# Kernel tuning notes

Hardware: AMD Instinct MI355X
Metric: run time of the kernel (lower is better)

Reference implementation:

```python
import jax, jax.numpy as jnp
import numpy as np

N_WIRES = 8
EMBED = 768
B, S = 16, 2048


def setup_inputs() -> dict:
    key = jax.random.key(0)
    k1, k2, k3, k4 = jax.random.split(key, 4)
    return {
        "x": jax.random.normal(k1, (B, S, EMBED), dtype=jnp.float32),
        "w_q": jax.random.normal(k2, (N_WIRES, EMBED), dtype=jnp.float32) * (1.0 / np.sqrt(EMBED)),
        "w_out": jax.random.normal(k3, (EMBED, N_WIRES), dtype=jnp.float32) * (1.0 / np.sqrt(N_WIRES)),
        "q_params": jax.random.normal(k4, (N_WIRES,), dtype=jnp.float32),
    }


def _simulate(angles):
    """Statevector sim: RX(angle_w) on each wire w, then ring of CNOTs, then <Z_w>.
    angles: [B, S, n].  Returns [B, S, n] Pauli-Z expectations."""
    b, s, n = angles.shape
    # |0...0> initial state, one qubit per trailing axis of size 2
    state = jnp.zeros((b, s) + (2,) * n, dtype=jnp.complex64)
    state = state.at[(slice(None), slice(None)) + (0,) * n].set(1.0)
    # RX gates (data angle + learned angle already fused in `angles`)
    for w in range(n):
        ax = 2 + w
        half = angles[..., w] * 0.5
        bshape = (b, s) + (1,) * (n - 1)
        c = jnp.cos(half).reshape(bshape)
        si = jnp.sin(half).reshape(bshape)
        a0 = jnp.take(state, 0, axis=ax)
        a1 = jnp.take(state, 1, axis=ax)
        state = jnp.stack([c * a0 - 1j * si * a1, -1j * si * a0 + c * a1], axis=ax)
    # CNOT chain: (0,1),(1,2),...,(n-2,n-1),(n-1,0)
    for src, tgt in [(i, i + 1) for i in range(n - 1)] + [(n - 1, 0)]:
        sax, tax = 2 + src, 2 + tgt
        a0 = jnp.take(state, 0, axis=sax)
        a1 = jnp.take(state, 1, axis=sax)
        tadj = tax - (1 if tax > sax else 0)  # target axis after removing src axis
        state = jnp.stack([a0, jnp.flip(a1, axis=tadj)], axis=sax)
    probs = jnp.real(state * jnp.conj(state))  # [B,S,2,...,2]
    zs = []
    for w in range(n):
        axes = tuple(a for a in range(2, 2 + n) if a != 2 + w)
        marg = probs.sum(axis=axes)  # [B,S,2]
        zs.append(marg[..., 0] - marg[..., 1])
    return jnp.stack(zs, axis=-1)


def reference(x, w_q, w_out, q_params):
    # per-token RX angles; two RX on same wire commute -> fuse data + learned angle
    angles = jnp.einsum("bse,ne->bsn", x, w_q) + q_params  # [B,S,n]
    z = _simulate(angles)  # [B,S,n]
    return jnp.einsum("bsn,en->bse", z, w_out)  # [B,S,E]
```

## Files before the change

kernel.cpp:

```cpp
#include <hip/hip_runtime.h>
#include <math.h>


using f32x4 = __attribute__((ext_vector_type(4))) float;

constexpr int E  = 768;
constexpr int NW = 8;
constexpr int BLOCK = 256;
constexpr int TOKENS = 16 * 2048;
constexpr int TOK_PER_WAVE  = 4;
constexpr int TOK_PER_BLOCK = TOK_PER_WAVE * 4;
constexpr int GRID = TOKENS / TOK_PER_BLOCK;

__device__ __forceinline__ float dot12(const f32x4& a0, const f32x4& a1, const f32x4& a2,
                                       const f32x4& b0, const f32x4& b1, const f32x4& b2) {
    return a0.x*b0.x + a0.y*b0.y + a0.z*b0.z + a0.w*b0.w
         + a1.x*b1.x + a1.y*b1.y + a1.z*b1.z + a1.w*b1.w
         + a2.x*b2.x + a2.y*b2.y + a2.z*b2.z + a2.w*b2.w;
}

__device__ __forceinline__ void circuit8(const float zf[NW], int lane, float qpl,
                                         float z[NW]) {
    float v4[4];
    #pragma unroll
    for (int i = 0; i < 4; ++i) {
        float a = zf[2*i], b = zf[2*i+1];
        float keep = (lane & 1) ? b : a;
        float send = (lane & 1) ? a : b;
        v4[i] = keep + __shfl_xor(send, 1, 64);
    }
    float v2[2];
    #pragma unroll
    for (int i = 0; i < 2; ++i) {
        float a = v4[2*i], b = v4[2*i+1];
        float keep = (lane & 2) ? b : a;
        float send = (lane & 2) ? a : b;
        v2[i] = keep + __shfl_xor(send, 2, 64);
    }
    float a = v2[0], b = v2[1];
    float keep = (lane & 4) ? b : a;
    float send = (lane & 4) ? a : b;
    float v = keep + __shfl_xor(send, 4, 64);
    v += __shfl_xor(v, 8, 64);
    v += __shfl_xor(v, 16, 64);
    v += __shfl_xor(v, 32, 64);
    float c = __cosf(v + qpl);
    float cx = __shfl_xor(c, 1, 64);
    float e0 = (lane & 1) ? cx : c;
    float e1 = (lane & 1) ? c : cx;
    float e0x = __shfl_xor(e0, 2, 64), e1x = __shfl_xor(e1, 2, 64);
    float f0 = (lane & 2) ? e0x : e0;
    float f1 = (lane & 2) ? e1x : e1;
    float f2 = (lane & 2) ? e0  : e0x;
    float f3 = (lane & 2) ? e1  : e1x;
    float f0x = __shfl_xor(f0, 4, 64), f1x = __shfl_xor(f1, 4, 64);
    float f2x = __shfl_xor(f2, 4, 64), f3x = __shfl_xor(f3, 4, 64);
    float c0 = (lane & 4) ? f0x : f0;
    float c1 = (lane & 4) ? f1x : f1;
    float c2 = (lane & 4) ? f2x : f2;
    float c3 = (lane & 4) ? f3x : f3;
    float c4 = (lane & 4) ? f0  : f0x;
    float c5 = (lane & 4) ? f1  : f1x;
    float c6 = (lane & 4) ? f2  : f2x;
    float c7 = (lane & 4) ? f3  : f3x;
    float p1 = c0*c1, p2 = p1*c2, p3 = p2*c3, p4 = p3*c4;
    float p5 = p4*c5, p6 = p5*c6, p7 = p6*c7;
    float s  = c1*c2*c3*c4*c5*c6*c7;
    z[0] = s;  z[1] = p1; z[2] = p2; z[3] = p3;
    z[4] = p4; z[5] = p5; z[6] = p6; z[7] = p7;
}

__global__ __launch_bounds__(BLOCK, 4)
void mhaq_kernel(const float* __restrict__ x,
                 const float* __restrict__ w_q,
                 const float* __restrict__ w_out,
                 const float* __restrict__ q_params,
                 float* __restrict__ out)
{
    __shared__ float wq_lds[NW][E];
    __shared__ float wt_lds[NW][E];

    const int tid  = threadIdx.x;
    const int wave = tid >> 6;
    const int lane = tid & 63;
    const int col  = lane * 4;
    const int t0   = blockIdx.x * TOK_PER_BLOCK + wave * TOK_PER_WAVE;

    f32x4 xv[TOK_PER_WAVE][3];
    #pragma unroll
    for (int tt = 0; tt < TOK_PER_WAVE; ++tt) {
        const f32x4* xp = reinterpret_cast<const f32x4*>(x + (size_t)(t0 + tt) * E);
        #pragma unroll
        for (int k = 0; k < 3; ++k)
            xv[tt][k] = xp[lane + k * 64];
    }

    {
        const f32x4* src = reinterpret_cast<const f32x4*>(w_q);
        f32x4* dst = reinterpret_cast<f32x4*>(&wq_lds[0][0]);
        #pragma unroll
        for (int r = 0; r < (NW * E / 4) / BLOCK; ++r)
            dst[tid + r * BLOCK] = src[tid + r * BLOCK];
    }
    {
        const f32x4* src = reinterpret_cast<const f32x4*>(w_out);
        #pragma unroll
        for (int r = 0; r < (NW * E / 4) / BLOCK; ++r) {
            int idx = tid + r * BLOCK;
            f32x4 v = src[idx];
            int e  = idx >> 1;
            int n0 = (idx & 1) * 4;
            wt_lds[n0 + 0][e] = v.x;
            wt_lds[n0 + 1][e] = v.y;
            wt_lds[n0 + 2][e] = v.z;
            wt_lds[n0 + 3][e] = v.w;
        }
    }
    const float qpl = q_params[lane & 7];
    __syncthreads();

    float zf[TOK_PER_WAVE][NW];
    #pragma unroll
    for (int n = 0; n < NW; ++n) {
        const f32x4 w0 = *reinterpret_cast<const f32x4*>(&wq_lds[n][col]);
        const f32x4 w1 = *reinterpret_cast<const f32x4*>(&wq_lds[n][col + 256]);
        const f32x4 w2 = *reinterpret_cast<const f32x4*>(&wq_lds[n][col + 512]);
        #pragma unroll
        for (int tt = 0; tt < TOK_PER_WAVE; ++tt)
            zf[tt][n] = dot12(xv[tt][0], xv[tt][1], xv[tt][2], w0, w1, w2);
    }

    float z[TOK_PER_WAVE][NW];
    #pragma unroll
    for (int tt = 0; tt < TOK_PER_WAVE; ++tt)
        circuit8(zf[tt], lane, qpl, z[tt]);

    #pragma unroll
    for (int k = 0; k < 3; ++k) {
        const int e0 = k * 256 + col;
        f32x4 wv[NW];
        #pragma unroll
        for (int n = 0; n < NW; ++n)
            wv[n] = *reinterpret_cast<const f32x4*>(&wt_lds[n][e0]);
        #pragma unroll
        for (int tt = 0; tt < TOK_PER_WAVE; ++tt) {
            float ox = 0.f, oy = 0.f, oz = 0.f, ow = 0.f;
            #pragma unroll
            for (int n = 0; n < NW; ++n) {
                ox += z[tt][n] * wv[n].x;
                oy += z[tt][n] * wv[n].y;
                oz += z[tt][n] * wv[n].z;
                ow += z[tt][n] * wv[n].w;
            }
            f32x4 o; o.x = ox; o.y = oy; o.z = oz; o.w = ow;
            *reinterpret_cast<f32x4*>(out + (size_t)(t0 + tt) * E + e0) = o;
        }
    }
}

extern "C" void kernel_launch(void* const* d_in, const int* in_sizes, int n_in,
                              void* d_out, int out_size, void* d_ws, size_t ws_size,
                              hipStream_t stream) {
    const float* x        = (const float*)d_in[0];
    const float* w_q      = (const float*)d_in[1];
    const float* w_out    = (const float*)d_in[2];
    const float* q_params = (const float*)d_in[3];
    float* out = (float*)d_out;

    hipLaunchKernelGGL(mhaq_kernel, dim3(GRID), dim3(BLOCK), 0, stream,
                       x, w_q, w_out, q_params, out);
}
```

Baseline: 36.36 us.

## Split per-wave tokens into two halves and overlap second load with first compute

Each wave now loads only two tokens of x up front, runs the projection, and then issues the loads for the remaining two tokens. Those loads are in flight while the first pair's circuit and output projection run. The aim is to lower register pressure and overlap global-memory latency with compute in this memory-bound kernel. The cost is fewer loads in flight at kernel start, which could hurt bandwidth utilisation.

```diff
diff --git a/kernel.cpp b/kernel.cpp
--- a/kernel.cpp
+++ b/kernel.cpp
@@ -70,6 +70,61 @@
     z[4] = p4; z[5] = p5; z[6] = p6; z[7] = p7;
 }
 
+__device__ __forceinline__ void load_x2(const float* __restrict__ x, int t0, int lane,
+                                        f32x4 xv[2][3]) {
+    #pragma unroll
+    for (int tt = 0; tt < 2; ++tt) {
+        const f32x4* xp = reinterpret_cast<const f32x4*>(x + (size_t)(t0 + tt) * E);
+        #pragma unroll
+        for (int k = 0; k < 3; ++k)
+            xv[tt][k] = xp[lane + k * 64];
+    }
+}
+
+__device__ __forceinline__ void dot2(const f32x4 xv[2][3], const float (*wq)[E], int col,
+                                     float zf[2][NW]) {
+    #pragma unroll
+    for (int n = 0; n < NW; ++n) {
+        const f32x4 w0 = *reinterpret_cast<const f32x4*>(&wq[n][col]);
+        const f32x4 w1 = *reinterpret_cast<const f32x4*>(&wq[n][col + 256]);
+        const f32x4 w2 = *reinterpret_cast<const f32x4*>(&wq[n][col + 512]);
+        #pragma unroll
+        for (int tt = 0; tt < 2; ++tt)
+            zf[tt][n] = dot12(xv[tt][0], xv[tt][1], xv[tt][2], w0, w1, w2);
+    }
+}
+
+__device__ __forceinline__ void finish2(float zf[2][NW], const float (*wt)[E],
+                                        int t0, int lane, int col, float qpl,
+                                        float* __restrict__ out) {
+    float z[2][NW];
+    #pragma unroll
+    for (int tt = 0; tt < 2; ++tt)
+        circuit8(zf[tt], lane, qpl, z[tt]);
+
+    #pragma unroll
+    for (int k = 0; k < 3; ++k) {
+        const int e0 = k * 256 + col;
+        f32x4 wv[NW];
+        #pragma unroll
+        for (int n = 0; n < NW; ++n)
+            wv[n] = *reinterpret_cast<const f32x4*>(&wt[n][e0]);
+        #pragma unroll
+        for (int tt = 0; tt < 2; ++tt) {
+            float ox = 0.f, oy = 0.f, oz = 0.f, ow = 0.f;
+            #pragma unroll
+            for (int n = 0; n < NW; ++n) {
+                ox += z[tt][n] * wv[n].x;
+                oy += z[tt][n] * wv[n].y;
+                oz += z[tt][n] * wv[n].z;
+                ow += z[tt][n] * wv[n].w;
+            }
+            f32x4 o; o.x = ox; o.y = oy; o.z = oz; o.w = ow;
+            *reinterpret_cast<f32x4*>(out + (size_t)(t0 + tt) * E + e0) = o;
+        }
+    }
+}
+
 __global__ __launch_bounds__(BLOCK, 4)
 void mhaq_kernel(const float* __restrict__ x,
                  const float* __restrict__ w_q,
@@ -86,14 +141,8 @@
     const int col  = lane * 4;
     const int t0   = blockIdx.x * TOK_PER_BLOCK + wave * TOK_PER_WAVE;
 
-    f32x4 xv[TOK_PER_WAVE][3];
-    #pragma unroll
-    for (int tt = 0; tt < TOK_PER_WAVE; ++tt) {
-        const f32x4* xp = reinterpret_cast<const f32x4*>(x + (size_t)(t0 + tt) * E);
-        #pragma unroll
-        for (int k = 0; k < 3; ++k)
-            xv[tt][k] = xp[lane + k * 64];
-    }
+    f32x4 xa[2][3];
+    load_x2(x, t0, lane, xa);
 
     {
         const f32x4* src = reinterpret_cast<const f32x4*>(w_q);
@@ -119,43 +168,17 @@
     const float qpl = q_params[lane & 7];
     __syncthreads();
 
-    float zf[TOK_PER_WAVE][NW];
-    #pragma unroll
-    for (int n = 0; n < NW; ++n) {
-        const f32x4 w0 = *reinterpret_cast<const f32x4*>(&wq_lds[n][col]);
-        const f32x4 w1 = *reinterpret_cast<const f32x4*>(&wq_lds[n][col + 256]);
-        const f32x4 w2 = *reinterpret_cast<const f32x4*>(&wq_lds[n][col + 512]);
-        #pragma unroll
-        for (int tt = 0; tt < TOK_PER_WAVE; ++tt)
-            zf[tt][n] = dot12(xv[tt][0], xv[tt][1], xv[tt][2], w0, w1, w2);
-    }
+    float zfa[2][NW];
+    dot2(xa, wq_lds, col, zfa);
 
-    float z[TOK_PER_WAVE][NW];
-    #pragma unroll
-    for (int tt = 0; tt < TOK_PER_WAVE; ++tt)
-        circuit8(zf[tt], lane, qpl, z[tt]);
+    f32x4 xb[2][3];
+    load_x2(x, t0 + 2, lane, xb);
 
-    #pragma unroll
-    for (int k = 0; k < 3; ++k) {
-        const int e0 = k * 256 + col;
-        f32x4 wv[NW];
-        #pragma unroll
-        for (int n = 0; n < NW; ++n)
-            wv[n] = *reinterpret_cast<const f32x4*>(&wt_lds[n][e0]);
-        #pragma unroll
-        for (int tt = 0; tt < TOK_PER_WAVE; ++tt) {
-            float ox = 0.f, oy = 0.f, oz = 0.f, ow = 0.f;
-            #pragma unroll
-            for (int n = 0; n < NW; ++n) {
-                ox += z[tt][n] * wv[n].x;
-                oy += z[tt][n] * wv[n].y;
-                oz += z[tt][n] * wv[n].z;
-                ow += z[tt][n] * wv[n].w;
-            }
-            f32x4 o; o.x = ox; o.y = oy; o.z = oz; o.w = ow;
-            *reinterpret_cast<f32x4*>(out + (size_t)(t0 + tt) * E + e0) = o;
-        }
-    }
+    finish2(zfa, wt_lds, t0, lane, col, qpl, out);
+
+    float zfb[2][NW];
+    dot2(xb, wq_lds, col, zfb);
+    finish2(zfb, wt_lds, t0 + 2, lane, col, qpl, out);
 }
 
 extern "C" void kernel_launch(void* const* d_in, const int* in_sizes, int n_in,
```

Result: slower. 37.41 us (+2.9%).

## Make blocks persistent over multiple token groups with double-buffered x prefetch

Applied to the files above, without the earlier changes.

Fixes the grid at 512 blocks, each looping over several 16-token groups. The w_q and w_out staging into LDS now happens once per block instead of once per 16 tokens, and the next group's x rows are prefetched into registers while the current group is finished. This cuts repeated weight staging and overlaps global loads with compute. In exchange it raises register pressure from the double buffer and reduces the number of blocks available to hide latency.

```diff
diff --git a/kernel.cpp b/kernel.cpp
--- a/kernel.cpp
+++ b/kernel.cpp
@@ -10,7 +10,8 @@
 constexpr int TOKENS = 16 * 2048;
 constexpr int TOK_PER_WAVE  = 4;
 constexpr int TOK_PER_BLOCK = TOK_PER_WAVE * 4;
-constexpr int GRID = TOKENS / TOK_PER_BLOCK;
+constexpr int GRID  = 512;
+constexpr int ITERS = TOKENS / (GRID * TOK_PER_BLOCK);
 
 __device__ __forceinline__ float dot12(const f32x4& a0, const f32x4& a1, const f32x4& a2,
                                        const f32x4& b0, const f32x4& b1, const f32x4& b2) {
@@ -70,6 +71,63 @@
     z[4] = p4; z[5] = p5; z[6] = p6; z[7] = p7;
 }
 
+__device__ __forceinline__ void load_x4(const float* __restrict__ x, int t0, int lane,
+                                        f32x4 xv[TOK_PER_WAVE][3]) {
+    #pragma unroll
+    for (int tt = 0; tt < TOK_PER_WAVE; ++tt) {
+        const f32x4* xp = reinterpret_cast<const f32x4*>(x + (size_t)(t0 + tt) * E);
+        #pragma unroll
+        for (int k = 0; k < 3; ++k)
+            xv[tt][k] = xp[lane + k * 64];
+    }
+}
+
+__device__ __forceinline__ void dot4(const f32x4 xv[TOK_PER_WAVE][3],
+                                     const float (*wq)[E], int col,
+                                     float zf[TOK_PER_WAVE][NW]) {
+    #pragma unroll
+    for (int n = 0; n < NW; ++n) {
+        const f32x4 w0 = *reinterpret_cast<const f32x4*>(&wq[n][col]);
+        const f32x4 w1 = *reinterpret_cast<const f32x4*>(&wq[n][col + 256]);
+        const f32x4 w2 = *reinterpret_cast<const f32x4*>(&wq[n][col + 512]);
+        #pragma unroll
+        for (int tt = 0; tt < TOK_PER_WAVE; ++tt)
+            zf[tt][n] = dot12(xv[tt][0], xv[tt][1], xv[tt][2], w0, w1, w2);
+    }
+}
+
+__device__ __forceinline__ void finish4(float zf[TOK_PER_WAVE][NW],
+                                        const float (*wt)[E],
+                                        int t0, int lane, int col, float qpl,
+                                        float* __restrict__ out) {
+    float z[TOK_PER_WAVE][NW];
+    #pragma unroll
+    for (int tt = 0; tt < TOK_PER_WAVE; ++tt)
+        circuit8(zf[tt], lane, qpl, z[tt]);
+
+    #pragma unroll
+    for (int k = 0; k < 3; ++k) {
+        const int e0 = k * 256 + col;
+        f32x4 wv[NW];
+        #pragma unroll
+        for (int n = 0; n < NW; ++n)
+            wv[n] = *reinterpret_cast<const f32x4*>(&wt[n][e0]);
+        #pragma unroll
+        for (int tt = 0; tt < TOK_PER_WAVE; ++tt) {
+            float ox = 0.f, oy = 0.f, oz = 0.f, ow = 0.f;
+            #pragma unroll
+            for (int n = 0; n < NW; ++n) {
+                ox += z[tt][n] * wv[n].x;
+                oy += z[tt][n] * wv[n].y;
+                oz += z[tt][n] * wv[n].z;
+                ow += z[tt][n] * wv[n].w;
+            }
+            f32x4 o; o.x = ox; o.y = oy; o.z = oz; o.w = ow;
+            *reinterpret_cast<f32x4*>(out + (size_t)(t0 + tt) * E + e0) = o;
+        }
+    }
+}
+
 __global__ __launch_bounds__(BLOCK, 4)
 void mhaq_kernel(const float* __restrict__ x,
                  const float* __restrict__ w_q,
@@ -84,16 +142,10 @@
     const int wave = tid >> 6;
     const int lane = tid & 63;
     const int col  = lane * 4;
-    const int t0   = blockIdx.x * TOK_PER_BLOCK + wave * TOK_PER_WAVE;
+    const int tbase = blockIdx.x * (TOK_PER_BLOCK * ITERS) + wave * TOK_PER_WAVE;
 
-    f32x4 xv[TOK_PER_WAVE][3];
-    #pragma unroll
-    for (int tt = 0; tt < TOK_PER_WAVE; ++tt) {
-        const f32x4* xp = reinterpret_cast<const f32x4*>(x + (size_t)(t0 + tt) * E);
-        #pragma unroll
-        for (int k = 0; k < 3; ++k)
-            xv[tt][k] = xp[lane + k * 64];
-    }
+    f32x4 xbuf[2][TOK_PER_WAVE][3];
+    load_x4(x, tbase, lane, xbuf[0]);
 
     {
         const f32x4* src = reinterpret_cast<const f32x4*>(w_q);
@@ -119,42 +171,14 @@
     const float qpl = q_params[lane & 7];
     __syncthreads();
 
-    float zf[TOK_PER_WAVE][NW];
     #pragma unroll
-    for (int n = 0; n < NW; ++n) {
-        const f32x4 w0 = *reinterpret_cast<const f32x4*>(&wq_lds[n][col]);
-        const f32x4 w1 = *reinterpret_cast<const f32x4*>(&wq_lds[n][col + 256]);
-        const f32x4 w2 = *reinterpret_cast<const f32x4*>(&wq_lds[n][col + 512]);
-        #pragma unroll
-        for (int tt = 0; tt < TOK_PER_WAVE; ++tt)
-            zf[tt][n] = dot12(xv[tt][0], xv[tt][1], xv[tt][2], w0, w1, w2);
-    }
-
-    float z[TOK_PER_WAVE][NW];
-    #pragma unroll
-    for (int tt = 0; tt < TOK_PER_WAVE; ++tt)
-        circuit8(zf[tt], lane, qpl, z[tt]);
-
-    #pragma unroll
-    for (int k = 0; k < 3; ++k) {
-        const int e0 = k * 256 + col;
-        f32x4 wv[NW];
-        #pragma unroll
-        for (int n = 0; n < NW; ++n)
-            wv[n] = *reinterpret_cast<const f32x4*>(&wt_lds[n][e0]);
-        #pragma unroll
-        for (int tt = 0; tt < TOK_PER_WAVE; ++tt) {
-            float ox = 0.f, oy = 0.f, oz = 0.f, ow = 0.f;
-            #pragma unroll
-            for (int n = 0; n < NW; ++n) {
-                ox += z[tt][n] * wv[n].x;
-                oy += z[tt][n] * wv[n].y;
-                oz += z[tt][n] * wv[n].z;
-                ow += z[tt][n] * wv[n].w;
-            }
-            f32x4 o; o.x = ox; o.y = oy; o.z = oz; o.w = ow;
-            *reinterpret_cast<f32x4*>(out + (size_t)(t0 + tt) * E + e0) = o;
-        }
+    for (int it = 0; it < ITERS; ++it) {
+        const int t0 = tbase + it * TOK_PER_BLOCK;
+        float zf[TOK_PER_WAVE][NW];
+        dot4(xbuf[it & 1], wq_lds, col, zf);
+        if (it + 1 < ITERS)
+            load_x4(x, t0 + TOK_PER_BLOCK, lane, xbuf[(it + 1) & 1]);
+        finish4(zf, wt_lds, t0, lane, col, qpl, out);
     }
 }
 
```

Measured after the change: 37.42 us. 2.9% more time.

## Make kernel persistent with double-buffered async global-to-LDS prefetch of x

Applied to the files above, without the earlier changes.

Turns the one-shot grid into a persistent grid of 256 blocks. Each block processes 8 iterations of 16 tokens. The x rows for the next iteration are prefetched straight into a double-buffered LDS area with global_load_lds, and an s_waitcnt vmcnt fence replaces the direct register loads. The goal is to load the weights once per block and overlap x fetches with compute and stores. The cost is about 146KB of LDS per block, so only one 4-wave block fits per CU, which lowers occupancy and limits latency hiding for this memory-bound kernel.

```diff
diff --git a/kernel.cpp b/kernel.cpp
--- a/kernel.cpp
+++ b/kernel.cpp
@@ -8,9 +8,10 @@
 constexpr int NW = 8;
 constexpr int BLOCK = 256;
 constexpr int TOKENS = 16 * 2048;
-constexpr int TOK_PER_WAVE  = 4;
-constexpr int TOK_PER_BLOCK = TOK_PER_WAVE * 4;
-constexpr int GRID = TOKENS / TOK_PER_BLOCK;
+constexpr int TOK_PER_WAVE = 4;
+constexpr int TOK_PER_ITER = 16;
+constexpr int GRID  = 256;
+constexpr int ITERS = TOKENS / (GRID * TOK_PER_ITER);
 
 __device__ __forceinline__ float dot12(const f32x4& a0, const f32x4& a1, const f32x4& a2,
                                        const f32x4& b0, const f32x4& b1, const f32x4& b2) {
@@ -70,7 +71,7 @@
     z[4] = p4; z[5] = p5; z[6] = p6; z[7] = p7;
 }
 
-__global__ __launch_bounds__(BLOCK, 4)
+__global__ __launch_bounds__(BLOCK, 1)
 void mhaq_kernel(const float* __restrict__ x,
                  const float* __restrict__ w_q,
                  const float* __restrict__ w_out,
@@ -79,20 +80,23 @@
 {
     __shared__ float wq_lds[NW][E];
     __shared__ float wt_lds[NW][E];
+    __shared__ float xb[2][TOK_PER_ITER][E];
 
     const int tid  = threadIdx.x;
     const int wave = tid >> 6;
     const int lane = tid & 63;
     const int col  = lane * 4;
-    const int t0   = blockIdx.x * TOK_PER_BLOCK + wave * TOK_PER_WAVE;
-
-    f32x4 xv[TOK_PER_WAVE][3];
-    #pragma unroll
-    for (int tt = 0; tt < TOK_PER_WAVE; ++tt) {
-        const f32x4* xp = reinterpret_cast<const f32x4*>(x + (size_t)(t0 + tt) * E);
-        #pragma unroll
-        for (int k = 0; k < 3; ++k)
-            xv[tt][k] = xp[lane + k * 64];
+    const int tblk = blockIdx.x * (TOK_PER_ITER * ITERS);
+
+    {
+        const float* src = x + (size_t)(tblk + 4 * wave) * E;
+        float* dst = &xb[0][4 * wave][0];
+        #pragma unroll
+        for (int i = 0; i < 12; ++i)
+            __builtin_amdgcn_global_load_lds(
+                (const __attribute__((address_space(1))) void*)(src + i * 256 + lane * 4),
+                (__attribute__((address_space(3))) void*)(dst + i * 256),
+                16, 0, 0);
     }
 
     {
@@ -119,41 +123,68 @@
     const float qpl = q_params[lane & 7];
     __syncthreads();
 
-    float zf[TOK_PER_WAVE][NW];
-    #pragma unroll
-    for (int n = 0; n < NW; ++n) {
-        const f32x4 w0 = *reinterpret_cast<const f32x4*>(&wq_lds[n][col]);
-        const f32x4 w1 = *reinterpret_cast<const f32x4*>(&wq_lds[n][col + 256]);
-        const f32x4 w2 = *reinterpret_cast<const f32x4*>(&wq_lds[n][col + 512]);
+    #pragma unroll 1
+    for (int it = 0; it < ITERS; ++it) {
+        if (it + 1 < ITERS) {
+            const float* src = x + (size_t)(tblk + (it + 1) * TOK_PER_ITER + 4 * wave) * E;
+            float* dst = &xb[(it + 1) & 1][4 * wave][0];
+            #pragma unroll
+            for (int i = 0; i < 12; ++i)
+                __builtin_amdgcn_global_load_lds(
+                    (const __attribute__((address_space(1))) void*)(src + i * 256 + lane * 4),
+                    (__attribute__((address_space(3))) void*)(dst + i * 256),
+                    16, 0, 0);
+        }
+        asm volatile("s_waitcnt vmcnt(12)" ::: "memory");
+        __builtin_amdgcn_sched_barrier(0);
+
+        const int t0 = tblk + it * TOK_PER_ITER + 4 * wave;
+        const float (*xcur)[E] = xb[it & 1];
+
+        f32x4 xv[TOK_PER_WAVE][3];
+        #pragma unroll
+        for (int tt = 0; tt < TOK_PER_WAVE; ++tt) {
+            #pragma unroll
+            for (int k = 0; k < 3; ++k)
+                xv[tt][k] = *reinterpret_cast<const f32x4*>(&xcur[4 * wave + tt][k * 256 + col]);
+        }
+
+        float zf[TOK_PER_WAVE][NW];
+        #pragma unroll
+        for (int n = 0; n < NW; ++n) {
+            const f32x4 w0 = *reinterpret_cast<const f32x4*>(&wq_lds[n][col]);
+            const f32x4 w1 = *reinterpret_cast<const f32x4*>(&wq_lds[n][col + 256]);
+            const f32x4 w2 = *reinterpret_cast<const f32x4*>(&wq_lds[n][col + 512]);
+            #pragma unroll
+            for (int tt = 0; tt < TOK_PER_WAVE; ++tt)
+                zf[tt][n] = dot12(xv[tt][0], xv[tt][1], xv[tt][2], w0, w1, w2);
+        }
+
+        float z[TOK_PER_WAVE][NW];
         #pragma unroll
         for (int tt = 0; tt < TOK_PER_WAVE; ++tt)
-            zf[tt][n] = dot12(xv[tt][0], xv[tt][1], xv[tt][2], w0, w1, w2);
-    }
-
-    float z[TOK_PER_WAVE][NW];
-    #pragma unroll
-    for (int tt = 0; tt < TOK_PER_WAVE; ++tt)
-        circuit8(zf[tt], lane, qpl, z[tt]);
-
-    #pragma unroll
-    for (int k = 0; k < 3; ++k) {
-        const int e0 = k * 256 + col;
-        f32x4 wv[NW];
-        #pragma unroll
-        for (int n = 0; n < NW; ++n)
-            wv[n] = *reinterpret_cast<const f32x4*>(&wt_lds[n][e0]);
-        #pragma unroll
-        for (int tt = 0; tt < TOK_PER_WAVE; ++tt) {
-            float ox = 0.f, oy = 0.f, oz = 0.f, ow = 0.f;
-            #pragma unroll
-            for (int n = 0; n < NW; ++n) {
-                ox += z[tt][n] * wv[n].x;
-                oy += z[tt][n] * wv[n].y;
-                oz += z[tt][n] * wv[n].z;
-                ow += z[tt][n] * wv[n].w;
+            circuit8(zf[tt], lane, qpl, z[tt]);
+
+        #pragma unroll
+        for (int k = 0; k < 3; ++k) {
+            const int e0 = k * 256 + col;
+            f32x4 wv[NW];
+            #pragma unroll
+            for (int n = 0; n < NW; ++n)
+                wv[n] = *reinterpret_cast<const f32x4*>(&wt_lds[n][e0]);
+            #pragma unroll
+            for (int tt = 0; tt < TOK_PER_WAVE; ++tt) {
+                float ox = 0.f, oy = 0.f, oz = 0.f, ow = 0.f;
+                #pragma unroll
+                for (int n = 0; n < NW; ++n) {
+                    ox += z[tt][n] * wv[n].x;
+                    oy += z[tt][n] * wv[n].y;
+                    oz += z[tt][n] * wv[n].z;
+                    ow += z[tt][n] * wv[n].w;
+                }
+                f32x4 o; o.x = ox; o.y = oy; o.z = oz; o.w = ow;
+                *reinterpret_cast<f32x4*>(out + (size_t)(t0 + tt) * E + e0) = o;
             }
-            f32x4 o; o.x = ox; o.y = oy; o.z = oz; o.w = ow;
-            *reinterpret_cast<f32x4*>(out + (size_t)(t0 + tt) * E + e0) = o;
         }
     }
 }
```

Result: slower. 42.37 us (+16.5%).
